# Kernel tuning notes

Hardware: AMD Instinct MI355X
Metric: run time of the kernel (lower is better)

Reference implementation:

```python
import jax, jax.numpy as jnp
import numpy as np

EMB = 128
B = 1024          # number of graphs (segments)
N = 500000        # total nodes
NEG_SLOPE = 0.01  # torch LeakyReLU default


def leaky_relu(v):
    return jnp.where(v >= 0, v, NEG_SLOPE * v)


def setup_inputs() -> dict:
    key = jax.random.key(0)
    ks = jax.random.split(key, 9)
    xg_old = jax.random.normal(ks[0], (B, EMB), dtype=jnp.float32)
    x = jax.random.normal(ks[1], (N, EMB), dtype=jnp.float32)
    batch = jnp.sort(jax.random.randint(ks[2], (N,), 0, B)).astype(jnp.int64)
    s = 1.0 / np.sqrt(EMB)
    w_mask = jax.random.uniform(ks[3], (EMB, 1), jnp.float32, -s, s)
    b_mask = jax.random.uniform(ks[4], (1,), jnp.float32, -s, s)
    w_feat = jax.random.uniform(ks[5], (EMB, EMB), jnp.float32, -s, s)
    b_feat = jax.random.uniform(ks[6], (EMB,), jnp.float32, -s, s)
    s2 = 1.0 / np.sqrt(2 * EMB)
    w_tr = jax.random.uniform(ks[7], (2 * EMB, EMB), jnp.float32, -s2, s2)
    b_tr = jax.random.uniform(ks[8], (EMB,), jnp.float32, -s2, s2)
    return {"xg_old": xg_old, "x": x, "batch": batch,
            "w_mask": w_mask, "b_mask": b_mask,
            "w_feat": w_feat, "b_feat": b_feat,
            "w_tr": w_tr, "b_tr": b_tr}


def reference(xg_old, x, batch, w_mask, b_mask, w_feat, b_feat, w_tr, b_tr):
    batch = batch.astype(jnp.int32)
    # gate score per node, segment-stable softmax over each graph
    gate = (x @ w_mask + b_mask)[:, 0]                        # [N]
    m = jax.ops.segment_max(gate, batch, num_segments=B)      # [B]
    e = jnp.exp(gate - m[batch])                              # [N]
    denom = jax.ops.segment_sum(e, batch, num_segments=B)     # [B]
    alpha = e / denom[batch]                                  # [N]
    # transformed node features, weighted segment-sum pooling
    feat = leaky_relu(x @ w_feat + b_feat)                    # [N, EMB]
    xg = jax.ops.segment_sum(alpha[:, None] * feat, batch, num_segments=B)  # [B, EMB]
    # concat with old global state, linear + LeakyReLU, residual
    cat = jnp.concatenate([xg, xg_old], axis=1)               # [B, 2*EMB]
    out = leaky_relu(cat @ w_tr + b_tr) + xg_old              # [B, EMB]
    return out
```

## Files before the change

kernel.cpp:

```cpp
#include <hip/hip_runtime.h>

typedef __attribute__((ext_vector_type(8))) short short8;
typedef __attribute__((ext_vector_type(4))) float floatx4;

__device__ __forceinline__ float b2f(unsigned int u) { return __uint_as_float(u << 16); }
__device__ __forceinline__ unsigned short f2b(float f) {
    unsigned int u = __float_as_uint(f);
    return (unsigned short)((u + 0x7fffu + ((u >> 16) & 1u)) >> 16);
}

#define EMB 128
#define NN  500000
#define BB  1024
#define BM  128
#define LDX 136
#define WTR 144

__global__ void kdetect(const unsigned short* __restrict__ xr,
                        const int* __restrict__ braw, int* __restrict__ flags, int N)
{
    int lane = threadIdx.x;
    int good = 0;
#pragma unroll
    for (int j = 0; j < 4; ++j) {
        unsigned short u = xr[lane * 4 + j];
        unsigned e = (u >> 7) & 0xffu;
        if ((e >= 100u && e <= 140u) || u == 0) ++good;
    }
#pragma unroll
    for (int o = 1; o < 64; o <<= 1) good += __shfl_xor(good, o);
    if (lane == 0) {
        flags[0] = (good < 240) ? 1 : 0;
        flags[1] = (braw[N - 1] == 0 && braw[N - 2] != 0) ? 1 : 0;
    }
}

__global__ __launch_bounds__(256)
void kinit(float* __restrict__ denom, float* __restrict__ xg,
           unsigned short* __restrict__ wT, const void* __restrict__ w_feat_,
           const void* __restrict__ w_mask_, const int* __restrict__ flags)
{
    int i = blockIdx.x * 256 + threadIdx.x;
    if (i < BB) denom[i] = 0.f;
    if (i < BB * EMB) xg[i] = 0.f;
    if (i < WTR * EMB) {
        int n = i >> 7, k = i & 127;
        unsigned short v;
        if (n < 128) v = flags[0] ? f2b(((const float*)w_feat_)[k * EMB + n])
                                  : ((const unsigned short*)w_feat_)[k * EMB + n];
        else if (n == 128) v = flags[0] ? f2b(((const float*)w_mask_)[k])
                                        : ((const unsigned short*)w_mask_)[k];
        else v = 0;
        wT[i] = v;
    }
}

__global__ __launch_bounds__(256, 4)
void kmain(const void* __restrict__ x_, const int* __restrict__ braw,
           const void* __restrict__ bm_, const void* __restrict__ bf_,
           const unsigned short* __restrict__ wT, const int* __restrict__ flags,
           float* __restrict__ denom, float* __restrict__ xg, int N)
{
    __shared__ __align__(16) unsigned short xs[4][32 * LDX];
    __shared__ float se[BM];
    __shared__ int   sb[BM];

    int tid = threadIdx.x;
    int wave = tid >> 6, lane = tid & 63;
    int quad = lane >> 4, l16 = lane & 15;
    int woff = wave * 32;
    int n0 = blockIdx.x * BM + woff;
    bool f32  = flags[0] != 0;
    bool is64 = flags[1] != 0;
    unsigned short* xw = xs[wave];

    if (lane < 32) {
        int n = n0 + lane; int s = -1;
        if (n < N) { int v = is64 ? braw[2 * n] : braw[n]; if (v >= 0 && v < BB) s = v; }
        sb[woff + lane] = s;
    }

    if (f32) {
        const float* xf = (const float*)x_;
#pragma unroll
        for (int it = 0; it < 8; ++it) {
            int c = it * 64 + lane;
            int row = c >> 4, k8 = (c & 15) * 8;
            int n = n0 + row;
            uint4 o = make_uint4(0u, 0u, 0u, 0u);
            if (n < N) {
                const float* p = xf + (size_t)n * EMB + k8;
                float4 a = *(const float4*)p, b = *(const float4*)(p + 4);
                o.x = (unsigned)f2b(a.x) | ((unsigned)f2b(a.y) << 16);
                o.y = (unsigned)f2b(a.z) | ((unsigned)f2b(a.w) << 16);
                o.z = (unsigned)f2b(b.x) | ((unsigned)f2b(b.y) << 16);
                o.w = (unsigned)f2b(b.z) | ((unsigned)f2b(b.w) << 16);
            }
            *(uint4*)(xw + row * LDX + k8) = o;
        }
    } else {
        const unsigned short* xu = (const unsigned short*)x_;
#pragma unroll
        for (int it = 0; it < 8; ++it) {
            int c = it * 64 + lane;
            int row = c >> 4, k8 = (c & 15) * 8;
            int n = n0 + row;
            uint4 v = make_uint4(0u, 0u, 0u, 0u);
            if (n < N) v = *(const uint4*)(xu + (size_t)n * EMB + k8);
            *(uint4*)(xw + row * LDX + k8) = v;
        }
    }

    floatx4 zero = {0.f, 0.f, 0.f, 0.f};
    floatx4 acc[2][9];
#pragma unroll
    for (int rt = 0; rt < 2; ++rt)
#pragma unroll
        for (int ct = 0; ct < 9; ++ct) acc[rt][ct] = zero;

#pragma unroll
    for (int k0 = 0; k0 < EMB; k0 += 32) {
        short8 a0 = *(const short8*)(xw + l16 * LDX + k0 + quad * 8);
        short8 a1 = *(const short8*)(xw + (16 + l16) * LDX + k0 + quad * 8);
#pragma unroll
        for (int ct = 0; ct < 9; ++ct) {
            short8 bf = *(const short8*)(wT + (ct * 16 + l16) * EMB + k0 + quad * 8);
            acc[0][ct] = __builtin_amdgcn_mfma_f32_16x16x32_bf16(a0, bf, acc[0][ct], 0, 0, 0);
            acc[1][ct] = __builtin_amdgcn_mfma_f32_16x16x32_bf16(a1, bf, acc[1][ct], 0, 0, 0);
        }
    }

    if (l16 == 0) {
#pragma unroll
        for (int rt = 0; rt < 2; ++rt)
#pragma unroll
            for (int r = 0; r < 4; ++r)
                se[woff + rt * 16 + quad * 4 + r] = acc[rt][8][r];
    }

    float bm = f32 ? ((const float*)bm_)[0]
                   : b2f((unsigned int)((const unsigned short*)bm_)[0]);

    if (lane < 32) {
        int sv = sb[woff + lane];
        float g = se[woff + lane] + bm;
        float ev = (sv >= 0) ? __expf(fminf(g, 60.f)) : 0.f;
        se[woff + lane] = ev;
        float v = ev;
#pragma unroll
        for (int o = 1; o < 32; o <<= 1) {
            float u  = __shfl_up(v, o);
            int   su = __shfl_up(sv, o);
            if (lane >= o && su == sv) v += u;
        }
        int sn = __shfl_down(sv, 1);
        if (sv >= 0 && (lane == 31 || sn != sv)) atomicAdd(&denom[sv], v);
    }

    float bfv[8];
#pragma unroll
    for (int ct = 0; ct < 8; ++ct)
        bfv[ct] = f32 ? ((const float*)bf_)[ct * 16 + l16]
                      : b2f((unsigned int)((const unsigned short*)bf_)[ct * 16 + l16]);

    float er[2][4]; int sr[2][4];
#pragma unroll
    for (int rt = 0; rt < 2; ++rt)
#pragma unroll
        for (int r = 0; r < 4; ++r) {
            int lr = rt * 16 + quad * 4 + r;
            er[rt][r] = se[woff + lr];
            sr[rt][r] = sb[woff + lr];
        }

    int sF = sb[woff], sL = sb[woff + 31];
    if (sF == sL) {
        if (sF >= 0) {
#pragma unroll
            for (int ct = 0; ct < 8; ++ct) {
                float p = 0.f;
#pragma unroll
                for (int rt = 0; rt < 2; ++rt)
#pragma unroll
                    for (int r = 0; r < 4; ++r) {
                        float v = acc[rt][ct][r] + bfv[ct];
                        v = v >= 0.f ? v : 0.01f * v;
                        p += v * er[rt][r];
                    }
                p += __shfl_xor(p, 16);
                p += __shfl_xor(p, 32);
                if (quad == (ct & 3))
                    atomicAdd(&xg[sF * EMB + ct * 16 + l16], p);
            }
        }
    } else {
#pragma unroll
        for (int ct = 0; ct < 8; ++ct) {
            int col = ct * 16 + l16;
#pragma unroll
            for (int rt = 0; rt < 2; ++rt) {
                float a = 0.f; int cur = -1;
#pragma unroll
                for (int r = 0; r < 4; ++r) {
                    int s = sr[rt][r];
                    float v = acc[rt][ct][r] + bfv[ct];
                    v = v >= 0.f ? v : 0.01f * v;
                    v *= er[rt][r];
                    if (s != cur) {
                        if (cur >= 0) atomicAdd(&xg[cur * EMB + col], a);
                        a = 0.f; cur = s;
                    }
                    if (s >= 0) a += v;
                }
                if (cur >= 0) atomicAdd(&xg[cur * EMB + col], a);
            }
        }
    }
}

__global__ __launch_bounds__(128)
void kfinal(const float* __restrict__ xg, const float* __restrict__ denom,
            const void* __restrict__ xg_old_, const void* __restrict__ w_tr_,
            const void* __restrict__ b_tr_, const int* __restrict__ flags,
            void* __restrict__ out_)
{
    __shared__ float cat[2 * EMB];
    int b = blockIdx.x, j = threadIdx.x;
    bool f32 = flags[0] != 0;

    float d = denom[b];
    float xgv = xg[b * EMB + j];
    xgv = (d > 0.f) ? xgv / d : 0.f;
    if (xgv != xgv) xgv = 700.0f;
    cat[j] = xgv;
    float old = f32 ? ((const float*)xg_old_)[b * EMB + j]
                    : b2f((unsigned int)((const unsigned short*)xg_old_)[b * EMB + j]);
    cat[EMB + j] = old;
    __syncthreads();

    float acc = f32 ? ((const float*)b_tr_)[j]
                    : b2f((unsigned int)((const unsigned short*)b_tr_)[j]);
    if (f32) {
        const float* w = (const float*)w_tr_;
#pragma unroll 8
        for (int i = 0; i < 2 * EMB; ++i) acc = fmaf(cat[i], w[i * EMB + j], acc);
    } else {
        const unsigned short* w = (const unsigned short*)w_tr_;
#pragma unroll 8
        for (int i = 0; i < 2 * EMB; ++i) acc = fmaf(cat[i], b2f((unsigned int)w[i * EMB + j]), acc);
    }
    acc = acc >= 0.f ? acc : 0.01f * acc;
    acc += old;
    if (acc != acc) acc = 300.0f;

    if (f32) ((float*)out_)[b * EMB + j] = acc;
    else     ((unsigned short*)out_)[b * EMB + j] = f2b(acc);
}

extern "C" void kernel_launch(void* const* d_in, const int* in_sizes, int n_in,
                              void* d_out, int out_size, void* d_ws, size_t ws_size,
                              hipStream_t stream) {
    const void* xg_old = d_in[0];
    const void* x      = d_in[1];
    const int*  braw   = (const int*)d_in[2];
    const void* w_mask = d_in[3];
    const void* b_mask = d_in[4];
    const void* w_feat = d_in[5];
    const void* b_feat = d_in[6];
    const void* w_tr   = d_in[7];
    const void* b_tr   = d_in[8];

    const int N = NN;

    char* ws = (char*)d_ws;
    size_t off = 0;
    int*   flags = (int*)(ws + off);   off += 64;
    float* denom = (float*)(ws + off); off += (size_t)BB * 4;
    float* xg    = (float*)(ws + off); off += (size_t)BB * EMB * 4;
    unsigned short* wT = (unsigned short*)(ws + off); off += (size_t)WTR * EMB * 2;

    kdetect<<<1, 64, 0, stream>>>((const unsigned short*)x, braw, flags, N);
    kinit<<<(BB * EMB + 255) / 256, 256, 0, stream>>>(denom, xg, wT, w_feat, w_mask, flags);
    kmain<<<(N + BM - 1) / BM, 256, 0, stream>>>(x, braw, b_mask, b_feat, wT,
                                                 flags, denom, xg, N);
    kfinal<<<BB, 128, 0, stream>>>(xg, denom, xg_old, w_tr, b_tr, flags, d_out);
}
```

Baseline: 438.8 us.

## Load x fragments directly into registers and pre-swizzle weights into MFMA fragment order

Drops the LDS staging of each wave's 32-row x tile. Each lane now loads its MFMA A-fragments straight from global memory, converting fp32 to bf16 in registers. The projection weights are pre-permuted in kinit into per-(k-block, column-tile) fragment order, so each B-fragment is one contiguous 16-byte-per-lane load. Occupancy hint is lowered from 4 to 3 blocks to allow more registers for the 16 float4 prefetch buffers. The trade-off is strided global loads (each lane reads 4 chunks 128 B apart per row) instead of coalesced row loads, plus higher register pressure.

```diff
diff --git a/kernel.cpp b/kernel.cpp
--- a/kernel.cpp
+++ b/kernel.cpp
@@ -13,8 +13,7 @@
 #define NN  500000
 #define BB  1024
 #define BM  128
-#define LDX 136
-#define WTR 144
+#define NCT 9
 
 __global__ void kdetect(const unsigned short* __restrict__ xr,
                         const int* __restrict__ braw, int* __restrict__ flags, int N)
@@ -37,31 +36,33 @@
 
 __global__ __launch_bounds__(256)
 void kinit(float* __restrict__ denom, float* __restrict__ xg,
-           unsigned short* __restrict__ wT, const void* __restrict__ w_feat_,
+           unsigned short* __restrict__ wTf, const void* __restrict__ w_feat_,
            const void* __restrict__ w_mask_, const int* __restrict__ flags)
 {
     int i = blockIdx.x * 256 + threadIdx.x;
     if (i < BB) denom[i] = 0.f;
     if (i < BB * EMB) xg[i] = 0.f;
-    if (i < WTR * EMB) {
-        int n = i >> 7, k = i & 127;
-        unsigned short v;
-        if (n < 128) v = flags[0] ? f2b(((const float*)w_feat_)[k * EMB + n])
-                                  : ((const unsigned short*)w_feat_)[k * EMB + n];
+    if (i < 4 * NCT * 512) {
+        int blk = i >> 9, rem = i & 511;
+        int lane = rem >> 3, j = rem & 7;
+        int kk = blk / NCT, ct = blk - kk * NCT;
+        int n = ct * 16 + (lane & 15);
+        int k = kk * 32 + (lane >> 4) * 8 + j;
+        unsigned short v = 0;
+        if (n < 128)      v = flags[0] ? f2b(((const float*)w_feat_)[k * EMB + n])
+                                       : ((const unsigned short*)w_feat_)[k * EMB + n];
         else if (n == 128) v = flags[0] ? f2b(((const float*)w_mask_)[k])
                                         : ((const unsigned short*)w_mask_)[k];
-        else v = 0;
-        wT[i] = v;
-    }
-}
-
-__global__ __launch_bounds__(256, 4)
+        wTf[i] = v;
+    }
+}
+
+__global__ __launch_bounds__(256, 3)
 void kmain(const void* __restrict__ x_, const int* __restrict__ braw,
            const void* __restrict__ bm_, const void* __restrict__ bf_,
-           const unsigned short* __restrict__ wT, const int* __restrict__ flags,
+           const unsigned short* __restrict__ wTf, const int* __restrict__ flags,
            float* __restrict__ denom, float* __restrict__ xg, int N)
 {
-    __shared__ __align__(16) unsigned short xs[4][32 * LDX];
     __shared__ float se[BM];
     __shared__ int   sb[BM];
 
@@ -72,7 +73,6 @@
     int n0 = blockIdx.x * BM + woff;
     bool f32  = flags[0] != 0;
     bool is64 = flags[1] != 0;
-    unsigned short* xw = xs[wave];
 
     if (lane < 32) {
         int n = n0 + lane; int s = -1;
@@ -80,53 +80,68 @@
         sb[woff + lane] = s;
     }
 
+    short8 afr[2][4];
     if (f32) {
         const float* xf = (const float*)x_;
-#pragma unroll
-        for (int it = 0; it < 8; ++it) {
-            int c = it * 64 + lane;
-            int row = c >> 4, k8 = (c & 15) * 8;
-            int n = n0 + row;
-            uint4 o = make_uint4(0u, 0u, 0u, 0u);
+        float4 av[16];
+        float4 z = make_float4(0.f, 0.f, 0.f, 0.f);
+#pragma unroll
+        for (int i = 0; i < 16; ++i) av[i] = z;
+#pragma unroll
+        for (int rt = 0; rt < 2; ++rt) {
+            int n = n0 + rt * 16 + l16;
+            const float* p = xf + (size_t)n * EMB + quad * 8;
             if (n < N) {
-                const float* p = xf + (size_t)n * EMB + k8;
-                float4 a = *(const float4*)p, b = *(const float4*)(p + 4);
-                o.x = (unsigned)f2b(a.x) | ((unsigned)f2b(a.y) << 16);
-                o.y = (unsigned)f2b(a.z) | ((unsigned)f2b(a.w) << 16);
-                o.z = (unsigned)f2b(b.x) | ((unsigned)f2b(b.y) << 16);
-                o.w = (unsigned)f2b(b.z) | ((unsigned)f2b(b.w) << 16);
-            }
-            *(uint4*)(xw + row * LDX + k8) = o;
-        }
+#pragma unroll
+                for (int kk = 0; kk < 4; ++kk) {
+                    av[rt * 8 + kk * 2]     = *(const float4*)(p + kk * 32);
+                    av[rt * 8 + kk * 2 + 1] = *(const float4*)(p + kk * 32 + 4);
+                }
+            }
+        }
+#pragma unroll
+        for (int rt = 0; rt < 2; ++rt)
+#pragma unroll
+            for (int kk = 0; kk < 4; ++kk) {
+                float4 a = av[rt * 8 + kk * 2], b = av[rt * 8 + kk * 2 + 1];
+                short8 t;
+                t[0] = (short)f2b(a.x); t[1] = (short)f2b(a.y);
+                t[2] = (short)f2b(a.z); t[3] = (short)f2b(a.w);
+                t[4] = (short)f2b(b.x); t[5] = (short)f2b(b.y);
+                t[6] = (short)f2b(b.z); t[7] = (short)f2b(b.w);
+                afr[rt][kk] = t;
+            }
     } else {
         const unsigned short* xu = (const unsigned short*)x_;
-#pragma unroll
-        for (int it = 0; it < 8; ++it) {
-            int c = it * 64 + lane;
-            int row = c >> 4, k8 = (c & 15) * 8;
-            int n = n0 + row;
-            uint4 v = make_uint4(0u, 0u, 0u, 0u);
-            if (n < N) v = *(const uint4*)(xu + (size_t)n * EMB + k8);
-            *(uint4*)(xw + row * LDX + k8) = v;
+        short8 z8 = {0, 0, 0, 0, 0, 0, 0, 0};
+#pragma unroll
+        for (int rt = 0; rt < 2; ++rt) {
+            int n = n0 + rt * 16 + l16;
+            const unsigned short* p = xu + (size_t)n * EMB + quad * 8;
+#pragma unroll
+            for (int kk = 0; kk < 4; ++kk) afr[rt][kk] = z8;
+            if (n < N) {
+#pragma unroll
+                for (int kk = 0; kk < 4; ++kk)
+                    afr[rt][kk] = *(const short8*)(p + kk * 32);
+            }
         }
     }
 
     floatx4 zero = {0.f, 0.f, 0.f, 0.f};
-    floatx4 acc[2][9];
+    floatx4 acc[2][NCT];
 #pragma unroll
     for (int rt = 0; rt < 2; ++rt)
 #pragma unroll
-        for (int ct = 0; ct < 9; ++ct) acc[rt][ct] = zero;
-
-#pragma unroll
-    for (int k0 = 0; k0 < EMB; k0 += 32) {
-        short8 a0 = *(const short8*)(xw + l16 * LDX + k0 + quad * 8);
-        short8 a1 = *(const short8*)(xw + (16 + l16) * LDX + k0 + quad * 8);
-#pragma unroll
-        for (int ct = 0; ct < 9; ++ct) {
-            short8 bf = *(const short8*)(wT + (ct * 16 + l16) * EMB + k0 + quad * 8);
-            acc[0][ct] = __builtin_amdgcn_mfma_f32_16x16x32_bf16(a0, bf, acc[0][ct], 0, 0, 0);
-            acc[1][ct] = __builtin_amdgcn_mfma_f32_16x16x32_bf16(a1, bf, acc[1][ct], 0, 0, 0);
+        for (int ct = 0; ct < NCT; ++ct) acc[rt][ct] = zero;
+
+#pragma unroll
+    for (int kk = 0; kk < 4; ++kk) {
+#pragma unroll
+        for (int ct = 0; ct < NCT; ++ct) {
+            short8 bf = *(const short8*)(wTf + ((kk * NCT + ct) << 9) + (lane << 3));
+            acc[0][ct] = __builtin_amdgcn_mfma_f32_16x16x32_bf16(afr[0][kk], bf, acc[0][ct], 0, 0, 0);
+            acc[1][ct] = __builtin_amdgcn_mfma_f32_16x16x32_bf16(afr[1][kk], bf, acc[1][ct], 0, 0, 0);
         }
     }
 
@@ -277,11 +292,11 @@
     int*   flags = (int*)(ws + off);   off += 64;
     float* denom = (float*)(ws + off); off += (size_t)BB * 4;
     float* xg    = (float*)(ws + off); off += (size_t)BB * EMB * 4;
-    unsigned short* wT = (unsigned short*)(ws + off); off += (size_t)WTR * EMB * 2;
+    unsigned short* wTf = (unsigned short*)(ws + off); off += (size_t)4 * NCT * 512 * 2;
 
     kdetect<<<1, 64, 0, stream>>>((const unsigned short*)x, braw, flags, N);
-    kinit<<<(BB * EMB + 255) / 256, 256, 0, stream>>>(denom, xg, wT, w_feat, w_mask, flags);
-    kmain<<<(N + BM - 1) / BM, 256, 0, stream>>>(x, braw, b_mask, b_feat, wT,
+    kinit<<<(BB * EMB + 255) / 256, 256, 0, stream>>>(denom, xg, wTf, w_feat, w_mask, flags);
+    kmain<<<(N + BM - 1) / BM, 256, 0, stream>>>(x, braw, b_mask, b_feat, wTf,
                                                  flags, denom, xg, N);
     kfinal<<<BB, 128, 0, stream>>>(xg, denom, xg_old, w_tr, b_tr, flags, d_out);
 }
```

Measured after the change: 404.5 us. 7.8% less time.
